# Kernel optimization log

Hardware: AMD Instinct MI355X
Metric: run time of the kernel (lower is better)

## Reference

```python
import jax, jax.numpy as jnp
import numpy as np

CH_IN, CH_OUT, IN_SIZE, CH_HID = 64, 64, 3, 32
LN_EPS = 1e-5


def _mlp(z, w1, b1, g, beta, w2, b2):
    # Linear -> LayerNorm -> ReLU -> Linear
    h = z @ w1.T + b1                       # [B, CH_HID]
    mu = jnp.mean(h, axis=-1, keepdims=True)
    var = jnp.var(h, axis=-1, keepdims=True)
    h = (h - mu) * jax.lax.rsqrt(var + LN_EPS) * g + beta
    h = jax.nn.relu(h)
    return h @ w2.T + b2


def setup_inputs() -> dict:
    key = jax.random.key(0)
    ks = jax.random.split(key, 10)
    B, T = 128, 4096
    def lin(k, fan_out, fan_in):
        bound = 1.0 / np.sqrt(fan_in)
        kw, kb = jax.random.split(k)
        return (jax.random.uniform(kw, (fan_out, fan_in), jnp.float32, -bound, bound),
                jax.random.uniform(kb, (fan_out,), jnp.float32, -bound, bound))
    w_w1, w_b1 = lin(ks[0], CH_HID, IN_SIZE)
    w_w2, w_b2 = lin(ks[1], CH_OUT * CH_IN, CH_HID)
    b_w1, b_b1 = lin(ks[2], CH_HID, IN_SIZE)
    b_w2, b_b2 = lin(ks[3], CH_OUT, CH_HID)
    return {
        "x": jax.random.normal(ks[4], (B, CH_IN, T), jnp.float32),
        "z": jax.random.normal(ks[5], (B, IN_SIZE), jnp.float32),
        "w_w1": w_w1, "w_b1": w_b1,
        "w_g": jnp.ones((CH_HID,), jnp.float32), "w_beta": jnp.zeros((CH_HID,), jnp.float32),
        "w_w2": w_w2, "w_b2": w_b2,
        "b_w1": b_w1, "b_b1": b_b1,
        "b_g": jnp.ones((CH_HID,), jnp.float32), "b_beta": jnp.zeros((CH_HID,), jnp.float32),
        "b_w2": b_w2, "b_b2": b_b2,
    }


def reference(x, z, w_w1, w_b1, w_g, w_beta, w_w2, w_b2,
              b_w1, b_b1, b_g, b_beta, b_w2, b_b2):
    B = x.shape[0]
    # hypernetwork: per-sample 1x1-conv weight [B, ch_out, ch_in] and bias [B, ch_out]
    weight = _mlp(z, w_w1, w_b1, w_g, w_beta, w_w2, w_b2).reshape(B, CH_OUT, CH_IN)
    bias = _mlp(z, b_w1, b_b1, b_g, b_beta, b_w2, b_b2)  # [B, CH_OUT]
    # grouped conv1d with kernel size 1 and groups=B == batched matmul
    out = jnp.einsum('boi,bit->bot', weight, x) + bias[:, :, None]
    return out
```

## Files before the change

### kernel.cpp

```cpp
#include <hip/hip_runtime.h>
#include <hip/hip_bf16.h>

#define B_SZ  128
#define CH    64
#define T_LEN 4096
#define HID   32
#define INS   3

#define PITCH  260
#define HALF_F 8384

typedef __attribute__((ext_vector_type(8))) short short8;
typedef __attribute__((ext_vector_type(4))) float f32x4;
typedef __attribute__((address_space(1))) const float gfloat1;
typedef __attribute__((address_space(3))) float sfloat3;

__device__ inline unsigned short f2bf_bits(float f) {
  __hip_bfloat16 h = __float2bfloat16(f);
  union { __hip_bfloat16 h; unsigned short u; } cv;
  cv.h = h;
  return cv.u;
}

__global__ __launch_bounds__(256) void hyper_mlp_kernel(
    const float* __restrict__ z,
    const float* __restrict__ w_w1, const float* __restrict__ w_b1,
    const float* __restrict__ w_g,  const float* __restrict__ w_beta,
    const float* __restrict__ w_w2, const float* __restrict__ w_b2,
    const float* __restrict__ b_w1, const float* __restrict__ b_b1,
    const float* __restrict__ b_g,  const float* __restrict__ b_beta,
    const float* __restrict__ b_w2, const float* __restrict__ b_b2,
    unsigned short* __restrict__ wbf,
    float* __restrict__ bias)
{
  const int blk = blockIdx.x;
  const int b   = blk >> 2;
  const int qt  = blk & 3;
  const int tid = threadIdx.x;

  __shared__ float zs[INS];
  __shared__ float hraw[2][HID];
  __shared__ float hn[2][HID];

  if (tid < INS) zs[tid] = z[b * INS + tid];
  __syncthreads();

  if (tid < 2 * HID) {
    const int grp = tid >> 5;
    const int j   = tid & 31;
    const float* w1 = grp ? b_w1 : w_w1;
    const float* b1 = grp ? b_b1 : w_b1;
    hraw[grp][j] = w1[j*3+0]*zs[0] + w1[j*3+1]*zs[1] + w1[j*3+2]*zs[2] + b1[j];
  }
  __syncthreads();

  if (tid < 2 * HID) {
    const int grp = tid >> 5;
    const int j   = tid & 31;
    float mu = 0.f;
    #pragma unroll
    for (int k = 0; k < HID; ++k) mu += hraw[grp][k];
    mu *= (1.0f / HID);
    float var = 0.f;
    #pragma unroll
    for (int k = 0; k < HID; ++k) { float d = hraw[grp][k] - mu; var += d * d; }
    var *= (1.0f / HID);
    const float r  = rsqrtf(var + 1e-5f);
    const float* g  = grp ? b_g    : w_g;
    const float* be = grp ? b_beta : w_beta;
    const float v = (hraw[grp][j] - mu) * r * g[j] + be[j];
    hn[grp][j] = fmaxf(v, 0.f);
  }
  __syncthreads();

  float h0[HID];
  #pragma unroll
  for (int j = 0; j < HID; ++j) h0[j] = hn[0][j];

  #pragma unroll
  for (int e = 0; e < 4; ++e) {
    const int m = qt * 1024 + e * 256 + tid;
    const float4* row = (const float4*)(w_w2 + (size_t)m * HID);
    float acc = w_b2[m];
    #pragma unroll
    for (int qq = 0; qq < 8; ++qq) {
      const float4 v = row[qq];
      acc += h0[qq*4+0] * v.x + h0[qq*4+1] * v.y
           + h0[qq*4+2] * v.z + h0[qq*4+3] * v.w;
    }
    wbf[(size_t)b * CH * CH + m] = f2bf_bits(acc);
  }

  if (qt == 0 && tid < CH) {
    const float4* row = (const float4*)(b_w2 + (size_t)tid * HID);
    float acc = b_b2[tid];
    #pragma unroll
    for (int qq = 0; qq < 8; ++qq) {
      const float4 v = row[qq];
      acc += hn[1][qq*4+0] * v.x + hn[1][qq*4+1] * v.y
           + hn[1][qq*4+2] * v.z + hn[1][qq*4+3] * v.w;
    }
    bias[b * CH + tid] = acc;
  }
}

#define STAGEH(H)                                                             \
  {                                                                           \
    _Pragma("unroll")                                                         \
    for (int q = 0; q < 8; ++q) {                                             \
      const int kp = wid * 8 + q;                        \
      const float* ga = xb + (size_t)(32 * (H) + kp) * T_LEN + lane * 4;      \
      __builtin_amdgcn_global_load_lds((gfloat1*)ga,                          \
          (sfloat3*)(lds + (H) * HALF_F + kp * PITCH + wid * 8), 16, 0, 0);   \
    }                                                                         \
  }

#define COMPKS(KS)                                                            \
  {                                                                           \
    _Pragma("unroll")                                                         \
    for (int nt = 0; nt < 4; ++nt) {                                          \
      union { short8 s; unsigned short u[8]; } bfv;                           \
      _Pragma("unroll")                                                       \
      for (int j = 0; j < 8; ++j) {                                           \
        const float f = lds[(KS) * HALF_F + (g * 8 + j) * PITCH + g * 8       \
                            + wid * 64 + nt * 16 + r];                        \
        bfv.u[j] = f2bf_bits(f);                                              \
      }                                                                       \
      acc[nt][0] = __builtin_amdgcn_mfma_f32_16x16x32_bf16(afrag[0][KS], bfv.s, acc[nt][0], 0, 0, 0); \
      acc[nt][1] = __builtin_amdgcn_mfma_f32_16x16x32_bf16(afrag[1][KS], bfv.s, acc[nt][1], 0, 0, 0); \
      acc[nt][2] = __builtin_amdgcn_mfma_f32_16x16x32_bf16(afrag[2][KS], bfv.s, acc[nt][2], 0, 0, 0); \
      acc[nt][3] = __builtin_amdgcn_mfma_f32_16x16x32_bf16(afrag[3][KS], bfv.s, acc[nt][3], 0, 0, 0); \
    }                                                                         \
  }

#define WAITB(N)                                                              \
  {                                                                           \
    asm volatile("s_waitcnt vmcnt(" #N ")" ::: "memory");                     \
    __builtin_amdgcn_s_barrier();                                             \
    asm volatile("" ::: "memory");                                            \
  }

#define LGKMB                                                                 \
  {                                                                           \
    asm volatile("s_waitcnt lgkmcnt(0)" ::: "memory");                        \
    __builtin_amdgcn_s_barrier();                                             \
    asm volatile("" ::: "memory");                                            \
  }

__global__ __launch_bounds__(256, 2) void conv1x1_mfma(
    const float* __restrict__ x,
    const unsigned short* __restrict__ wbf,
    const float* __restrict__ bias,
    float* __restrict__ out)
{
  __shared__ __align__(16) float lds[2 * HALF_F];

  const int b    = blockIdx.y;
  const int tbi  = blockIdx.x;
  const int tid  = threadIdx.x;
  const int lane = tid & 63;
  const int wid  = tid >> 6;
  const int g    = lane >> 4;
  const int r    = lane & 15;

  const unsigned short* wb = wbf + (size_t)b * CH * CH;
  short8 afrag[4][2];
  #pragma unroll
  for (int ot = 0; ot < 4; ++ot)
    #pragma unroll
    for (int ks = 0; ks < 2; ++ks)
      afrag[ot][ks] = *(const short8*)(wb + (ot * 16 + r) * CH + ks * 32 + g * 8);

  float bv[4][4];
  #pragma unroll
  for (int ot = 0; ot < 4; ++ot) {
    const float4 t = *(const float4*)(bias + b * CH + ot * 16 + g * 4);
    bv[ot][0] = t.x; bv[ot][1] = t.y; bv[ot][2] = t.z; bv[ot][3] = t.w;
  }

  const float* xb = x   + (size_t)b * CH * T_LEN + tbi * 256;
  float*       ob = out + (size_t)b * CH * T_LEN + tbi * 256;

  f32x4 acc[4][4];
  #pragma unroll
  for (int nt = 0; nt < 4; ++nt)
    #pragma unroll
    for (int ot = 0; ot < 4; ++ot) {
      f32x4 a = {bv[ot][0], bv[ot][1], bv[ot][2], bv[ot][3]};
      acc[nt][ot] = a;
    }

  STAGEH(0)
  STAGEH(1)

  WAITB(8)
  COMPKS(0)

  WAITB(0)
  COMPKS(1)

  LGKMB

  #pragma unroll
  for (int nt = 0; nt < 4; ++nt)
    #pragma unroll
    for (int ot = 0; ot < 4; ++ot)
      #pragma unroll
      for (int qq = 0; qq < 4; ++qq)
        lds[(ot * 16 + g * 4 + qq) * PITCH + wid * 64 + nt * 16 + r] =
            acc[nt][ot][qq];

  LGKMB

  #pragma unroll
  for (int j = 0; j < 16; ++j) {
    const int o = wid * 16 + j;
    const f32x4 v = *(const f32x4*)(&lds[o * PITCH + lane * 4]);
    __builtin_nontemporal_store(v, (f32x4*)(&ob[(size_t)o * T_LEN + lane * 4]));
  }
}

extern "C" void kernel_launch(void* const* d_in, const int* in_sizes, int n_in,
                              void* d_out, int out_size, void* d_ws, size_t ws_size,
                              hipStream_t stream) {
  const float* x      = (const float*)d_in[0];
  const float* z      = (const float*)d_in[1];
  const float* w_w1   = (const float*)d_in[2];
  const float* w_b1   = (const float*)d_in[3];
  const float* w_g    = (const float*)d_in[4];
  const float* w_beta = (const float*)d_in[5];
  const float* w_w2   = (const float*)d_in[6];
  const float* w_b2   = (const float*)d_in[7];
  const float* b_w1   = (const float*)d_in[8];
  const float* b_b1   = (const float*)d_in[9];
  const float* b_g    = (const float*)d_in[10];
  const float* b_beta = (const float*)d_in[11];
  const float* b_w2   = (const float*)d_in[12];
  const float* b_b2   = (const float*)d_in[13];

  float* out = (float*)d_out;
  unsigned short* wbf = (unsigned short*)d_ws;
  float* bias = (float*)((char*)d_ws + (size_t)B_SZ * CH * CH * sizeof(unsigned short));

  hyper_mlp_kernel<<<B_SZ * 4, 256, 0, stream>>>(
      z, w_w1, w_b1, w_g, w_beta, w_w2, w_b2,
      b_w1, b_b1, b_g, b_beta, b_w2, b_b2, wbf, bias);

  dim3 grid(T_LEN / 256, B_SZ);
  conv1x1_mfma<<<grid, 256, 0, stream>>>(x, wbf, bias, out);
}
```

Before: 59.40 us.

## Halve conv time tile to 128 and pack channel pairs per LDS row

The conv kernel now processes 128 time steps per block instead of 256. It packs two channels per LDS row with a new pitch, which cuts LDS use to about 34 KB and raises the launch-bounds occupancy hint from 2 to 4 blocks. The two-stage split load with a partial wait is replaced by one load followed by a full wait, giving more blocks and more waves in flight to hide memory latency. In exchange, each block now loads its per-sample weight fragments and bias for half as much output, so that overhead doubles per byte processed, and the intra-block overlap of load and compute is lost.

Measured after the change: 58.39 us. No clear change (-1.7%).

```diff
diff --git a/kernel.cpp b/kernel.cpp
--- a/kernel.cpp
+++ b/kernel.cpp
@@ -7,8 +7,7 @@
 #define HID   32
 #define INS   3
 
-#define PITCH  260
-#define HALF_F 8384
+#define PPITCH 268
 
 typedef __attribute__((ext_vector_type(8))) short short8;
 typedef __attribute__((ext_vector_type(4))) float f32x4;
@@ -104,35 +103,6 @@
   }
 }
 
-#define STAGEH(H)                                                             \
-  {                                                                           \
-    _Pragma("unroll")                                                         \
-    for (int q = 0; q < 8; ++q) {                                             \
-      const int kp = wid * 8 + q;                        \
-      const float* ga = xb + (size_t)(32 * (H) + kp) * T_LEN + lane * 4;      \
-      __builtin_amdgcn_global_load_lds((gfloat1*)ga,                          \
-          (sfloat3*)(lds + (H) * HALF_F + kp * PITCH + wid * 8), 16, 0, 0);   \
-    }                                                                         \
-  }
-
-#define COMPKS(KS)                                                            \
-  {                                                                           \
-    _Pragma("unroll")                                                         \
-    for (int nt = 0; nt < 4; ++nt) {                                          \
-      union { short8 s; unsigned short u[8]; } bfv;                           \
-      _Pragma("unroll")                                                       \
-      for (int j = 0; j < 8; ++j) {                                           \
-        const float f = lds[(KS) * HALF_F + (g * 8 + j) * PITCH + g * 8       \
-                            + wid * 64 + nt * 16 + r];                        \
-        bfv.u[j] = f2bf_bits(f);                                              \
-      }                                                                       \
-      acc[nt][0] = __builtin_amdgcn_mfma_f32_16x16x32_bf16(afrag[0][KS], bfv.s, acc[nt][0], 0, 0, 0); \
-      acc[nt][1] = __builtin_amdgcn_mfma_f32_16x16x32_bf16(afrag[1][KS], bfv.s, acc[nt][1], 0, 0, 0); \
-      acc[nt][2] = __builtin_amdgcn_mfma_f32_16x16x32_bf16(afrag[2][KS], bfv.s, acc[nt][2], 0, 0, 0); \
-      acc[nt][3] = __builtin_amdgcn_mfma_f32_16x16x32_bf16(afrag[3][KS], bfv.s, acc[nt][3], 0, 0, 0); \
-    }                                                                         \
-  }
-
 #define WAITB(N)                                                              \
   {                                                                           \
     asm volatile("s_waitcnt vmcnt(" #N ")" ::: "memory");                     \
@@ -147,13 +117,13 @@
     asm volatile("" ::: "memory");                                            \
   }
 
-__global__ __launch_bounds__(256, 2) void conv1x1_mfma(
+__global__ __launch_bounds__(256, 4) void conv1x1_mfma(
     const float* __restrict__ x,
     const unsigned short* __restrict__ wbf,
     const float* __restrict__ bias,
     float* __restrict__ out)
 {
-  __shared__ __align__(16) float lds[2 * HALF_F];
+  __shared__ __align__(16) float lds[32 * PPITCH];
 
   const int b    = blockIdx.y;
   const int tbi  = blockIdx.x;
@@ -178,45 +148,65 @@
     bv[ot][0] = t.x; bv[ot][1] = t.y; bv[ot][2] = t.z; bv[ot][3] = t.w;
   }
 
-  const float* xb = x   + (size_t)b * CH * T_LEN + tbi * 256;
-  float*       ob = out + (size_t)b * CH * T_LEN + tbi * 256;
-
-  f32x4 acc[4][4];
-  #pragma unroll
-  for (int nt = 0; nt < 4; ++nt)
+  const float* xb = x   + (size_t)b * CH * T_LEN + tbi * 128;
+  float*       ob = out + (size_t)b * CH * T_LEN + tbi * 128;
+
+  f32x4 acc[2][4];
+  #pragma unroll
+  for (int nt = 0; nt < 2; ++nt)
     #pragma unroll
     for (int ot = 0; ot < 4; ++ot) {
       f32x4 a = {bv[ot][0], bv[ot][1], bv[ot][2], bv[ot][3]};
       acc[nt][ot] = a;
     }
 
-  STAGEH(0)
-  STAGEH(1)
-
-  WAITB(8)
-  COMPKS(0)
+  #pragma unroll
+  for (int q = 0; q < 8; ++q) {
+    const int m = wid * 8 + q;
+    const float* ga = xb + (size_t)(2 * m + (lane >> 5)) * T_LEN + (lane & 31) * 4;
+    __builtin_amdgcn_global_load_lds((gfloat1*)ga,
+        (sfloat3*)(lds + m * PPITCH), 16, 0, 0);
+  }
 
   WAITB(0)
-  COMPKS(1)
+
+  #pragma unroll
+  for (int ks = 0; ks < 2; ++ks) {
+    #pragma unroll
+    for (int nt = 0; nt < 2; ++nt) {
+      union { short8 s; unsigned short u[8]; } bfv;
+      #pragma unroll
+      for (int j = 0; j < 8; ++j) {
+        const float f = lds[(ks * 16 + g * 4 + (j >> 1)) * PPITCH
+                            + (j & 1) * 128 + wid * 32 + nt * 16 + r];
+        bfv.u[j] = f2bf_bits(f);
+      }
+      acc[nt][0] = __builtin_amdgcn_mfma_f32_16x16x32_bf16(afrag[0][ks], bfv.s, acc[nt][0], 0, 0, 0);
+      acc[nt][1] = __builtin_amdgcn_mfma_f32_16x16x32_bf16(afrag[1][ks], bfv.s, acc[nt][1], 0, 0, 0);
+      acc[nt][2] = __builtin_amdgcn_mfma_f32_16x16x32_bf16(afrag[2][ks], bfv.s, acc[nt][2], 0, 0, 0);
+      acc[nt][3] = __builtin_amdgcn_mfma_f32_16x16x32_bf16(afrag[3][ks], bfv.s, acc[nt][3], 0, 0, 0);
+    }
+  }
 
   LGKMB
 
   #pragma unroll
-  for (int nt = 0; nt < 4; ++nt)
+  for (int nt = 0; nt < 2; ++nt)
     #pragma unroll
     for (int ot = 0; ot < 4; ++ot)
       #pragma unroll
       for (int qq = 0; qq < 4; ++qq)
-        lds[(ot * 16 + g * 4 + qq) * PITCH + wid * 64 + nt * 16 + r] =
-            acc[nt][ot][qq];
+        lds[(ot * 8 + g * 2 + (qq >> 1)) * PPITCH + (qq & 1) * 128
+            + wid * 32 + nt * 16 + r] = acc[nt][ot][qq];
 
   LGKMB
 
   #pragma unroll
-  for (int j = 0; j < 16; ++j) {
-    const int o = wid * 16 + j;
-    const f32x4 v = *(const f32x4*)(&lds[o * PITCH + lane * 4]);
-    __builtin_nontemporal_store(v, (f32x4*)(&ob[(size_t)o * T_LEN + lane * 4]));
+  for (int s = 0; s < 8; ++s) {
+    const int p = wid * 8 + s;
+    const f32x4 v = *(const f32x4*)(&lds[p * PPITCH + (lane >> 5) * 128 + (lane & 31) * 4]);
+    __builtin_nontemporal_store(v,
+        (f32x4*)(&ob[(size_t)(2 * p + (lane >> 5)) * T_LEN + (lane & 31) * 4]));
   }
 }
 
@@ -246,6 +236,6 @@
       z, w_w1, w_b1, w_g, w_beta, w_w2, w_b2,
       b_w1, b_b1, b_g, b_beta, b_w2, b_b2, wbf, bias);
 
-  dim3 grid(T_LEN / 256, B_SZ);
+  dim3 grid(T_LEN / 128, B_SZ);
   conv1x1_mfma<<<grid, 256, 0, stream>>>(x, wbf, bias, out);
 }
```
